# Performance work log

Measured on AMD Instinct MI355X. Metric: run time of the kernel, lower is better.

Reference implementation:

```python
import jax, jax.numpy as jnp
import numpy as np

B, N, C, HEADS = 8, 1024, 768, 12
HW = 32  # H = W = 32, so H*W == N


def _layernorm(x, g, b, eps=1e-5):
    mu = x.mean(-1, keepdims=True)
    var = ((x - mu) ** 2).mean(-1, keepdims=True)
    return (x - mu) * jax.lax.rsqrt(var + eps) * g + b


def setup_inputs() -> dict:
    key = jax.random.key(0)
    ks = jax.random.split(key, 6)
    w = lambda k, shape: jax.random.normal(k, shape, dtype=jnp.float32) * 0.02
    return {
        "x": jax.random.normal(ks[0], (B, N, C), dtype=jnp.float32),
        "y": jax.random.normal(ks[1], (B, C, HW, HW), dtype=jnp.float32),
        "q_w": w(ks[2], (C, C)),
        "q_b": jnp.zeros((C,), jnp.float32),
        "kv_w": w(ks[3], (2 * C, C)),
        "kv_b": jnp.zeros((2 * C,), jnp.float32),
        "proj_w": w(ks[4], (C, C)),
        "proj_b": jnp.zeros((C,), jnp.float32),
        "ln_g": jnp.ones((C,), jnp.float32),
        "ln_b": jnp.zeros((C,), jnp.float32),
        "H": HW,
        "W": HW,
    }


def reference(x, y, q_w, q_b, kv_w, kv_b, proj_w, proj_b, ln_g, ln_b, H, W):
    Bn, Nn, Cn = x.shape
    hd = Cn // HEADS
    scale = hd ** -0.5  # qk_scale=None, c_ratio=1 -> head_dim**-0.5

    # gating tensors from y
    y1 = y.reshape(Bn, Cn, H * W).transpose(0, 2, 1)          # [B, N, C]
    y2 = _layernorm(y1, ln_g, ln_b)
    yq = jax.nn.sigmoid(y2 @ q_w.T + q_b)                      # [B, N, C]
    ykv = jax.nn.sigmoid(y2 @ kv_w.T + kv_b)                   # [B, N, 2C]

    # gated q: q2 = q0 + q0*yq
    q0 = x @ q_w.T + q_b
    q = (q0 + q0 * yq).reshape(Bn, Nn, HEADS, hd).transpose(0, 2, 1, 3)  # [B,h,N,d]

    # gated kv: kv2 = kv0*ykv + ykv
    kv0 = x @ kv_w.T + kv_b
    kv = (kv0 * ykv + ykv).reshape(Bn, Nn, 2, HEADS, hd).transpose(2, 0, 3, 1, 4)
    k, v = kv[0], kv[1]                                        # [B,h,N,d] each

    attn = jax.nn.softmax(jnp.einsum("bhqd,bhkd->bhqk", q, k) * scale, axis=-1)
    out = jnp.einsum("bhqk,bhkd->bhqd", attn, v)
    out = out.transpose(0, 2, 1, 3).reshape(Bn, Nn, Cn)
    return out @ proj_w.T + proj_b
```

## Files before the change

kernel.cpp:

```cpp
#include <hip/hip_runtime.h>
#include <stdint.h>

typedef __attribute__((ext_vector_type(4))) float f4;
typedef __attribute__((ext_vector_type(8))) short bf16x8;
typedef __attribute__((ext_vector_type(4))) unsigned short u16x4;
typedef unsigned short u16;

#define B_ 8
#define N_ 1024
#define C_ 768
#define NH 12
#define HD 64

__device__ __forceinline__ float bf2f(u16 v) {
  union { unsigned u; float f; } x; x.u = ((unsigned)v) << 16; return x.f;
}
__device__ __forceinline__ u16 f2bf(float f) {
  union { float f; unsigned u; } x; x.f = f;
  unsigned r = x.u + 0x7FFFu + ((x.u >> 16) & 1u);
  return (u16)(r >> 16);
}
__device__ __forceinline__ void g2l16(const u16* g, const u16* l) {
  __builtin_amdgcn_global_load_lds(
      (const __attribute__((address_space(1))) void*)(uintptr_t)g,
      (__attribute__((address_space(3))) void*)(uint32_t)(uintptr_t)l,
      16, 0, 0);
}

#define SW6()  asm volatile("s_waitcnt vmcnt(6)" ::: "memory")
#define SW4()  asm volatile("s_waitcnt vmcnt(4)" ::: "memory")
#define SW3()  asm volatile("s_waitcnt vmcnt(3)" ::: "memory")
#define SW0()  asm volatile("s_waitcnt vmcnt(0)" ::: "memory")
#define BARF()                              \
  do {                                      \
    __builtin_amdgcn_s_barrier();           \
    asm volatile("" ::: "memory");          \
    __builtin_amdgcn_sched_barrier(0);      \
  } while (0)

__global__ __launch_bounds__(256) void cvt_bf16(const float* __restrict__ s,
                                                u16* __restrict__ d, int n4) {
  int i = blockIdx.x * 256 + threadIdx.x;
  int stride = gridDim.x * 256;
  for (; i < n4; i += stride) {
    float4 v = ((const float4*)s)[i];
    u16x4 o;
    o.x = f2bf(v.x); o.y = f2bf(v.y); o.z = f2bf(v.z); o.w = f2bf(v.w);
    ((u16x4*)d)[i] = o;
  }
}

__global__ __launch_bounds__(256) void ln_stats(const float* __restrict__ y,
                                                float* __restrict__ mu,
                                                float* __restrict__ rs,
                                                int b0) {
  __shared__ float s1[4][64], s2[4][64];
  int t = threadIdx.x;
  int nl = t & 63, ch = t >> 6;
  int idx0 = b0 * N_ + blockIdx.x * 64;
  int b = idx0 >> 10, nb_ = idx0 & 1023;
  const float* p = y + (size_t)b * C_ * N_ + nb_ + nl;
  float s = 0.f, q = 0.f;
  int c0 = ch * 192;
  for (int c = c0; c < c0 + 192; ++c) {
    float v = p[(size_t)c * N_];
    s += v; q += v * v;
  }
  s1[ch][nl] = s; s2[ch][nl] = q;
  __syncthreads();
  if (t < 64) {
    float ts = s1[0][t] + s1[1][t] + s1[2][t] + s1[3][t];
    float tq = s2[0][t] + s2[1][t] + s2[2][t] + s2[3][t];
    float m = ts * (1.f / C_);
    float var = tq * (1.f / C_) - m * m;
    mu[idx0 + t] = m;
    rs[idx0 + t] = rsqrtf(fmaxf(var, 0.f) + 1e-5f);
  }
}

__global__ __launch_bounds__(256) void ln_apply(const float* __restrict__ y,
                                                const float* __restrict__ mu,
                                                const float* __restrict__ rs,
                                                const float* __restrict__ lg,
                                                const float* __restrict__ lb,
                                                u16* __restrict__ y2c,
                                                int b0) {
  __shared__ float tile[64][65];
  int t = threadIdx.x;
  int n0 = blockIdx.x * 64, c0 = blockIdx.y * 64;
  int bl = blockIdx.z, b = b0 + bl;
  int jc = (t & 15) * 4, ir = t >> 4;
  for (int r = 0; r < 4; ++r) {
    int i = ir + r * 16;
    float4 v = *(const float4*)(y + ((size_t)b * C_ + c0 + i) * N_ + n0 + jc);
    tile[i][jc] = v.x; tile[i][jc + 1] = v.y; tile[i][jc + 2] = v.z; tile[i][jc + 3] = v.w;
  }
  __syncthreads();
  for (int r = 0; r < 4; ++r) {
    int i = ir + r * 16;
    int n = n0 + i;
    float m = mu[b * N_ + n], rr = rs[b * N_ + n];
    float g0 = lg[c0 + jc],     b0f = lb[c0 + jc];
    float g1 = lg[c0 + jc + 1], b1f = lb[c0 + jc + 1];
    float g2 = lg[c0 + jc + 2], b2f = lb[c0 + jc + 2];
    float g3 = lg[c0 + jc + 3], b3f = lb[c0 + jc + 3];
    u16x4 o;
    o.x = f2bf((tile[jc][i] - m) * rr * g0 + b0f);
    o.y = f2bf((tile[jc + 1][i] - m) * rr * g1 + b1f);
    o.z = f2bf((tile[jc + 2][i] - m) * rr * g2 + b2f);
    o.w = f2bf((tile[jc + 3][i] - m) * rr * g3 + b3f);
    *(u16x4*)(y2c + ((size_t)bl * N_ + n) * C_ + c0 + jc) = o;
  }
}

__global__ __launch_bounds__(256, 2) void gemm_gate(
    const u16* __restrict__ xbc, const u16* __restrict__ y2c,
    const u16* __restrict__ qwb, const u16* __restrict__ kvwb,
    const float* __restrict__ qb_, const float* __restrict__ kvb_,
    u16* __restrict__ o_q, u16* __restrict__ o_k, u16* __restrict__ o_vT) {
  __shared__ u16 smem[36864];
  int t = threadIdx.x, l = t & 63;
  int quad = l >> 4, l15 = l & 15;
  int w = t >> 6, wm = w & 1, wn = w >> 1;
  int m0l = blockIdx.x * 128;
  int n0l = blockIdx.y * 128;

  const u16* wp; const float* bp; int sel, h0;
  if (n0l < C_) {
    wp = qwb + (size_t)n0l * C_; bp = qb_ + n0l; sel = 0; h0 = n0l >> 6;
  } else {
    int nk = n0l - C_;
    wp = kvwb + (size_t)nk * C_; bp = kvb_ + nk;
    sel = (nk < C_) ? 1 : 2;
    h0 = ((sel == 2) ? nk - C_ : nk) >> 6;
  }

  f4 accx[4][4], accy[4][4];
  for (int i = 0; i < 4; ++i)
    for (int j = 0; j < 4; ++j) {
      accx[i][j] = (f4){0.f, 0.f, 0.f, 0.f};
      accy[i][j] = (f4){0.f, 0.f, 0.f, 0.f};
    }

  int row = t >> 2;
  int colS = (((t & 3) ^ (row & 3)) * 8);
  const u16* gx = xbc + (size_t)(m0l + row) * C_ + colS;
  const u16* gy = y2c + (size_t)(m0l + row) * C_ + colS;
  const u16* gw = wp + (size_t)row * C_ + colS;
  int rsl = (quad ^ (l15 & 3)) * 8;

#define STAGE_G(OFF, kk)                                   \
  do {                                                     \
    u16* p_ = smem + (OFF);                                \
    g2l16(gx + (kk),           p_ + t * 8);                \
    g2l16(gx + (kk) + 64 * C_, p_ + 2048 + t * 8);         \
    g2l16(gy + (kk),           p_ + 4096 + t * 8);         \
    g2l16(gy + (kk) + 64 * C_, p_ + 6144 + t * 8);         \
    g2l16(gw + (kk),           p_ + 8192 + t * 8);         \
    g2l16(gw + (kk) + 64 * C_, p_ + 10240 + t * 8);        \
  } while (0)

#define COMPUTE_G(OFF)                                                        \
  do {                                                                        \
    const u16* base = smem + (OFF);                                           \
    bf16x8 afx[4], afy[4], bfr[4];                                            \
    for (int i = 0; i < 4; ++i) {                                             \
      int ra = (wm * 64 + i * 16 + l15) * 32 + rsl;                           \
      afx[i] = *(const bf16x8*)&base[ra];                                     \
      afy[i] = *(const bf16x8*)&base[4096 + ra];                              \
      int rb = (wn * 64 + i * 16 + l15) * 32 + rsl;                           \
      bfr[i] = *(const bf16x8*)&base[8192 + rb];                              \
    }                                                                         \
    for (int i = 0; i < 4; ++i)                                               \
      for (int j = 0; j < 4; ++j) {                                           \
        accx[i][j] = __builtin_amdgcn_mfma_f32_16x16x32_bf16(afx[i], bfr[j], accx[i][j], 0, 0, 0); \
        accy[i][j] = __builtin_amdgcn_mfma_f32_16x16x32_bf16(afy[i], bfr[j], accy[i][j], 0, 0, 0); \
      }                                                                       \
  } while (0)

#define STEP_G(i, OFFC, OFFS)                                 \
  do {                                                        \
    if ((i) <= 21) STAGE_G(OFFS, ((i) + 2) * 32);             \
    COMPUTE_G(OFFC);                                          \
    if ((i) <= 21)      SW6();                                \
    else if ((i) == 22) SW0();                                \
    BARF();                                                   \
  } while (0)

  STAGE_G(0, 0);
  STAGE_G(12288, 32);
  SW6();
  BARF();
  for (int n = 0; n < 24; n += 3) {
    STEP_G(n,     0,     24576);
    STEP_G(n + 1, 12288, 0);
    STEP_G(n + 2, 24576, 12288);
  }
#undef STEP_G
#undef STAGE_G
#undef COMPUTE_G

  const int PITCH = 136;
  for (int j = 0; j < 4; ++j) {
    int cloc = wn * 64 + j * 16 + l15;
    float bias = bp[cloc];
    for (int i = 0; i < 4; ++i) {
      int rb0 = wm * 64 + i * 16 + quad * 4;
      for (int r = 0; r < 4; ++r) {
        int rloc = rb0 + r;
        float vx = accx[i][j][r] + bias;
        float vy = accy[i][j][r] + bias;
        float gg = 1.f / (1.f + __expf(-vy));
        float val = (sel == 0) ? vx * (1.f + gg) : gg * (vx + 1.f);
        u16 bv = f2bf(val);
        if (sel == 2) smem[cloc * PITCH + rloc] = bv;
        else          smem[rloc * PITCH + cloc] = bv;
      }
    }
  }
  __syncthreads();
  {
    int rr = t >> 1, hh = t & 1;
    const u16* src = smem + rr * PITCH + hh * 64;
    u16* dst;
    if (sel == 2) {
      int h = h0 + (rr >> 6), d = rr & 63;
      int bl = m0l >> 10, nbase = m0l & 1023;
      dst = o_vT + (size_t)((bl * NH + h) * HD + d) * N_ + nbase + hh * 64;
    } else {
      int gml = m0l + rr;
      int bl = gml >> 10, n = gml & 1023;
      int h = h0 + hh;
      dst = (sel == 0 ? o_q : o_k) + (size_t)((bl * NH + h) * N_ + n) * HD;
    }
    for (int c = 0; c < 8; ++c) {
      bf16x8 v = *(const bf16x8*)(src + c * 8);
      *(bf16x8*)(dst + c * 8) = v;
    }
  }
}

__global__ __launch_bounds__(256) void attn(const u16* __restrict__ qoc,
                                            const u16* __restrict__ koc,
                                            const u16* __restrict__ vTc,
                                            u16* __restrict__ aoc) {
  __shared__ u16 Qs[4096], Ks[8192], Vs[8192];
  __shared__ u16 Ps[64 * 72];
  int t = threadIdx.x, l = t & 63, w = t >> 6;
  int quad = l >> 4, l15 = l & 15;
  int bhl = blockIdx.y;
  int bl = bhl / NH, h = bhl % NH;
  int q0 = blockIdx.x * 64;
  int sr = t >> 3;
  int swo = ((t & 7) ^ (sr & 7)) * 8;
  const u16* qbp = qoc + ((size_t)bhl * N_ + q0) * HD;
  const u16* kb = koc + (size_t)bhl * N_ * HD;
  const u16* vb = vTc + (size_t)bhl * HD * N_;

#define STAGE_KV(OFF, key0)                                                   \
  do {                                                                        \
    g2l16(kb + (size_t)((key0) + sr) * HD + swo,      Ks + (OFF) + t * 8);    \
    g2l16(kb + (size_t)((key0) + 32 + sr) * HD + swo, Ks + (OFF) + 2048 + t * 8); \
    g2l16(vb + (size_t)sr * N_ + (key0) + swo,        Vs + (OFF) + t * 8);    \
    g2l16(vb + (size_t)(32 + sr) * N_ + (key0) + swo, Vs + (OFF) + 2048 + t * 8); \
  } while (0)

  g2l16(qbp + sr * HD + swo,        Qs + t * 8);
  g2l16(qbp + (32 + sr) * HD + swo, Qs + 2048 + t * 8);
  STAGE_KV(0, 0);
  STAGE_KV(4096, 64);
  SW4();
  BARF();

  int sA = (quad ^ (l15 & 7)) * 8;
  int sB = sA ^ 32;
  bf16x8 aq0 = *(const bf16x8*)&Qs[(w * 16 + l15) * 64 + sA];
  bf16x8 aq1 = *(const bf16x8*)&Qs[(w * 16 + l15) * 64 + sB];
  f4 o[4];
  for (int i = 0; i < 4; ++i) o[i] = (f4){0.f, 0.f, 0.f, 0.f};
  f4 ls = (f4){0.f, 0.f, 0.f, 0.f};
  bf16x8 ones;
  for (int i = 0; i < 8; ++i) ones[i] = (short)0x3F80;

#define TILE_STEP(KOFF)                                                       \
  do {                                                                        \
    f4 s_[4];                                                                 \
    __builtin_amdgcn_s_setprio(1);                                            \
    for (int ni = 0; ni < 4; ++ni) {                                          \
      bf16x8 b0v = *(const bf16x8*)&Ks[(KOFF) + (ni * 16 + l15) * 64 + sA];   \
      bf16x8 b1v = *(const bf16x8*)&Ks[(KOFF) + (ni * 16 + l15) * 64 + sB];   \
      f4 z = (f4){0.f, 0.f, 0.f, 0.f};                                        \
      z = __builtin_amdgcn_mfma_f32_16x16x32_bf16(aq0, b0v, z, 0, 0, 0);      \
      z = __builtin_amdgcn_mfma_f32_16x16x32_bf16(aq1, b1v, z, 0, 0, 0);      \
      s_[ni] = z;                                                             \
    }                                                                         \
    __builtin_amdgcn_s_setprio(0);                                            \
    for (int ni = 0; ni < 4; ++ni)                                            \
      for (int r = 0; r < 4; ++r)                                             \
        Ps[(w * 16 + quad * 4 + r) * 72 + ni * 16 + l15] =                    \
            f2bf(__expf(s_[ni][r] * 0.125f));                                 \
    bf16x8 ap0 = *(const bf16x8*)&Ps[(w * 16 + l15) * 72 + quad * 8];         \
    bf16x8 ap1 = *(const bf16x8*)&Ps[(w * 16 + l15) * 72 + 32 + quad * 8];    \
    __builtin_amdgcn_s_setprio(1);                                            \
    for (int ni = 0; ni < 4; ++ni) {                                          \
      bf16x8 b0v = *(const bf16x8*)&Vs[(KOFF) + (ni * 16 + l15) * 64 + sA];   \
      bf16x8 b1v = *(const bf16x8*)&Vs[(KOFF) + (ni * 16 + l15) * 64 + sB];   \
      o[ni] = __builtin_amdgcn_mfma_f32_16x16x32_bf16(ap0, b0v, o[ni], 0, 0, 0); \
      o[ni] = __builtin_amdgcn_mfma_f32_16x16x32_bf16(ap1, b1v, o[ni], 0, 0, 0); \
    }                                                                         \
    ls = __builtin_amdgcn_mfma_f32_16x16x32_bf16(ap0, ones, ls, 0, 0, 0);     \
    ls = __builtin_amdgcn_mfma_f32_16x16x32_bf16(ap1, ones, ls, 0, 0, 0);     \
    __builtin_amdgcn_s_setprio(0);                                            \
  } while (0)

  for (int kt = 0; kt < 16; kt += 2) {
    TILE_STEP(0);
    BARF();
    if (kt + 2 < 16) { STAGE_KV(0, (kt + 2) * 64); SW4(); } else { SW0(); }
    BARF();
    TILE_STEP(4096);
    BARF();
    if (kt + 3 < 16) { STAGE_KV(4096, (kt + 3) * 64); SW4(); } else { SW0(); }
    BARF();
  }
#undef TILE_STEP
#undef STAGE_KV

  for (int ni = 0; ni < 4; ++ni)
    for (int r = 0; r < 4; ++r)
      Ps[(w * 16 + quad * 4 + r) * 72 + ni * 16 + l15] =
          f2bf(o[ni][r] / ls[r]);
  __syncthreads();
  {
    int rr = t >> 2, cc = t & 3;
    int n = q0 + rr;
    const u16* src = Ps + rr * 72 + cc * 16;
    u16* dst = aoc + ((size_t)bl * N_ + n) * C_ + h * HD + cc * 16;
    *(bf16x8*)dst = *(const bf16x8*)src;
    *(bf16x8*)(dst + 8) = *(const bf16x8*)(src + 8);
  }
}

__global__ __launch_bounds__(256, 2) void gemm_proj(const u16* __restrict__ aoc,
                                                    const u16* __restrict__ pwb,
                                                    const float* __restrict__ bias,
                                                    float* __restrict__ out,
                                                    int b0) {
  __shared__ u16 smem[18432];
  int t = threadIdx.x, l = t & 63;
  int quad = l >> 4, l15 = l & 15;
  int w = t >> 6, wm = w & 1, wn = w >> 1;
  int m0l = blockIdx.x * 128, n0 = blockIdx.y * 64;
  f4 acc[4][2];
  for (int i = 0; i < 4; ++i)
    for (int j = 0; j < 2; ++j) acc[i][j] = (f4){0.f, 0.f, 0.f, 0.f};
  int row = t >> 2;
  int colS = (((t & 3) ^ (row & 3)) * 8);
  const u16* ga = aoc + (size_t)(m0l + row) * C_ + colS;
  const u16* gw = pwb + (size_t)(n0 + row) * C_ + colS;
  int rsl = (quad ^ (l15 & 3)) * 8;

#define STAGE_P(OFF, kk)                                   \
  do {                                                     \
    u16* p_ = smem + (OFF);                                \
    g2l16(ga + (kk),           p_ + t * 8);                \
    g2l16(ga + (kk) + 64 * C_, p_ + 2048 + t * 8);         \
    g2l16(gw + (kk),           p_ + 4096 + t * 8);         \
  } while (0)

#define COMPUTE_P(OFF)                                                        \
  do {                                                                        \
    const u16* base = smem + (OFF);                                           \
    bf16x8 af[4], bfr[2];                                                     \
    for (int i = 0; i < 4; ++i)                                               \
      af[i] = *(const bf16x8*)&base[(wm * 64 + i * 16 + l15) * 32 + rsl];     \
    for (int j = 0; j < 2; ++j)                                               \
      bfr[j] = *(const bf16x8*)&base[4096 + (wn * 32 + j * 16 + l15) * 32 + rsl]; \
    for (int i = 0; i < 4; ++i)                                               \
      for (int j = 0; j < 2; ++j)                                             \
        acc[i][j] = __builtin_amdgcn_mfma_f32_16x16x32_bf16(af[i], bfr[j], acc[i][j], 0, 0, 0); \
  } while (0)

#define STEP_P(i, OFFC, OFFS)                                 \
  do {                                                        \
    if ((i) <= 21) STAGE_P(OFFS, ((i) + 2) * 32);             \
    COMPUTE_P(OFFC);                                          \
    if ((i) <= 21)      SW3();                                \
    else if ((i) == 22) SW0();                                \
    BARF();                                                   \
  } while (0)

  STAGE_P(0, 0);
  STAGE_P(6144, 32);
  SW3();
  BARF();
  for (int n = 0; n < 24; n += 3) {
    STEP_P(n,     0,     12288);
    STEP_P(n + 1, 6144,  0);
    STEP_P(n + 2, 12288, 6144);
  }
#undef STEP_P
#undef STAGE_P
#undef COMPUTE_P

  for (int j = 0; j < 2; ++j) {
    int gcol = n0 + wn * 32 + j * 16 + l15;
    float bv = bias[gcol];
    for (int i = 0; i < 4; ++i) {
      int rbase = m0l + wm * 64 + i * 16 + quad * 4;
      for (int r = 0; r < 4; ++r)
        __builtin_nontemporal_store(acc[i][j][r] + bv,
                                    &out[(size_t)(b0 * N_ + rbase + r) * C_ + gcol]);
    }
  }
}

extern "C" void kernel_launch(void* const* d_in, const int* in_sizes, int n_in,
                              void* d_out, int out_size, void* d_ws, size_t ws_size,
                              hipStream_t stream) {
  const float* x   = (const float*)d_in[0];
  const float* y   = (const float*)d_in[1];
  const float* qw  = (const float*)d_in[2];
  const float* qb  = (const float*)d_in[3];
  const float* kvw = (const float*)d_in[4];
  const float* kvb = (const float*)d_in[5];
  const float* pw  = (const float*)d_in[6];
  const float* pb  = (const float*)d_in[7];
  const float* lg  = (const float*)d_in[8];
  const float* lb  = (const float*)d_in[9];

  char* ws = (char*)d_ws;
  float* mu = (float*)(ws);
  float* rs = (float*)(ws + 32768);
  u16* qwb  = (u16*)(ws + 65536);
  u16* kvwb = (u16*)(ws + 1245184);
  u16* pwb  = (u16*)(ws + 3604480);
  const size_t BASE2 = 4784128;
  const size_t PER_B = 1572864;

  int nb = 1;
  for (int c = 8; c >= 1; c >>= 1) {
    if (BASE2 + 5 * (size_t)c * PER_B <= ws_size) { nb = c; break; }
  }
  u16* xbc = (u16*)(ws + BASE2);
  u16* y2c = (u16*)(ws + BASE2 + (size_t)nb * PER_B);
  u16* qoc = (u16*)(ws + BASE2 + 2 * (size_t)nb * PER_B);
  u16* koc = (u16*)(ws + BASE2 + 3 * (size_t)nb * PER_B);
  u16* vTc = (u16*)(ws + BASE2 + 4 * (size_t)nb * PER_B);
  u16* aoc = xbc;

  cvt_bf16<<<dim3(576), dim3(256), 0, stream>>>(qw, qwb, 147456);
  cvt_bf16<<<dim3(1152), dim3(256), 0, stream>>>(kvw, kvwb, 294912);
  cvt_bf16<<<dim3(576), dim3(256), 0, stream>>>(pw, pwb, 147456);

  for (int b0 = 0; b0 < B_; b0 += nb) {
    cvt_bf16<<<dim3(768 * nb), dim3(256), 0, stream>>>(
        x + (size_t)b0 * N_ * C_, xbc, nb * 196608);
    ln_stats<<<dim3(16 * nb), dim3(256), 0, stream>>>(y, mu, rs, b0);
    ln_apply<<<dim3(16, 12, nb), dim3(256), 0, stream>>>(y, mu, rs, lg, lb, y2c, b0);
    gemm_gate<<<dim3(8 * nb, 18), dim3(256), 0, stream>>>(xbc, y2c, qwb, kvwb,
                                                          qb, kvb, qoc, koc, vTc);
    attn<<<dim3(16, 12 * nb), dim3(256), 0, stream>>>(qoc, koc, vTc, aoc);
    gemm_proj<<<dim3(8 * nb, 12), dim3(256), 0, stream>>>(aoc, pwb, pb, (float*)d_out, b0);
  }
}
```

Measured before the change: 285.5 us.

## Shrink gate GEMM N-tile to 64 and drop triple-buffered LDS pipeline

```diff
diff --git a/kernel.cpp b/kernel.cpp
--- a/kernel.cpp
+++ b/kernel.cpp
@@ -27,7 +27,6 @@
       16, 0, 0);
 }
 
-#define SW6()  asm volatile("s_waitcnt vmcnt(6)" ::: "memory")
 #define SW4()  asm volatile("s_waitcnt vmcnt(4)" ::: "memory")
 #define SW3()  asm volatile("s_waitcnt vmcnt(3)" ::: "memory")
 #define SW0()  asm volatile("s_waitcnt vmcnt(0)" ::: "memory")
@@ -113,17 +112,17 @@
   }
 }
 
-__global__ __launch_bounds__(256, 2) void gemm_gate(
+__global__ __launch_bounds__(256, 4) void gemm_gate(
     const u16* __restrict__ xbc, const u16* __restrict__ y2c,
     const u16* __restrict__ qwb, const u16* __restrict__ kvwb,
     const float* __restrict__ qb_, const float* __restrict__ kvb_,
     u16* __restrict__ o_q, u16* __restrict__ o_k, u16* __restrict__ o_vT) {
-  __shared__ u16 smem[36864];
+  __shared__ u16 smem[10240];
   int t = threadIdx.x, l = t & 63;
   int quad = l >> 4, l15 = l & 15;
   int w = t >> 6, wm = w & 1, wn = w >> 1;
   int m0l = blockIdx.x * 128;
-  int n0l = blockIdx.y * 128;
+  int n0l = blockIdx.y * 64;
 
   const u16* wp; const float* bp; int sel, h0;
   if (n0l < C_) {
@@ -135,74 +134,50 @@
     h0 = ((sel == 2) ? nk - C_ : nk) >> 6;
   }
 
-  f4 accx[4][4], accy[4][4];
+  f4 accx[4][2], accy[4][2];
   for (int i = 0; i < 4; ++i)
-    for (int j = 0; j < 4; ++j) {
+    for (int j = 0; j < 2; ++j) {
       accx[i][j] = (f4){0.f, 0.f, 0.f, 0.f};
       accy[i][j] = (f4){0.f, 0.f, 0.f, 0.f};
     }
 
-  int row = t >> 2;
-  int colS = (((t & 3) ^ (row & 3)) * 8);
-  const u16* gx = xbc + (size_t)(m0l + row) * C_ + colS;
-  const u16* gy = y2c + (size_t)(m0l + row) * C_ + colS;
-  const u16* gw = wp + (size_t)row * C_ + colS;
-  int rsl = (quad ^ (l15 & 3)) * 8;
-
-#define STAGE_G(OFF, kk)                                   \
-  do {                                                     \
-    u16* p_ = smem + (OFF);                                \
-    g2l16(gx + (kk),           p_ + t * 8);                \
-    g2l16(gx + (kk) + 64 * C_, p_ + 2048 + t * 8);         \
-    g2l16(gy + (kk),           p_ + 4096 + t * 8);         \
-    g2l16(gy + (kk) + 64 * C_, p_ + 6144 + t * 8);         \
-    g2l16(gw + (kk),           p_ + 8192 + t * 8);         \
-    g2l16(gw + (kk) + 64 * C_, p_ + 10240 + t * 8);        \
-  } while (0)
-
-#define COMPUTE_G(OFF)                                                        \
-  do {                                                                        \
-    const u16* base = smem + (OFF);                                           \
-    bf16x8 afx[4], afy[4], bfr[4];                                            \
-    for (int i = 0; i < 4; ++i) {                                             \
-      int ra = (wm * 64 + i * 16 + l15) * 32 + rsl;                           \
-      afx[i] = *(const bf16x8*)&base[ra];                                     \
-      afy[i] = *(const bf16x8*)&base[4096 + ra];                              \
-      int rb = (wn * 64 + i * 16 + l15) * 32 + rsl;                           \
-      bfr[i] = *(const bf16x8*)&base[8192 + rb];                              \
-    }                                                                         \
-    for (int i = 0; i < 4; ++i)                                               \
-      for (int j = 0; j < 4; ++j) {                                           \
-        accx[i][j] = __builtin_amdgcn_mfma_f32_16x16x32_bf16(afx[i], bfr[j], accx[i][j], 0, 0, 0); \
-        accy[i][j] = __builtin_amdgcn_mfma_f32_16x16x32_bf16(afy[i], bfr[j], accy[i][j], 0, 0, 0); \
-      }                                                                       \
-  } while (0)
-
-#define STEP_G(i, OFFC, OFFS)                                 \
-  do {                                                        \
-    if ((i) <= 21) STAGE_G(OFFS, ((i) + 2) * 32);             \
-    COMPUTE_G(OFFC);                                          \
-    if ((i) <= 21)      SW6();                                \
-    else if ((i) == 22) SW0();                                \
-    BARF();                                                   \
-  } while (0)
-
-  STAGE_G(0, 0);
-  STAGE_G(12288, 32);
-  SW6();
-  BARF();
-  for (int n = 0; n < 24; n += 3) {
-    STEP_G(n,     0,     24576);
-    STEP_G(n + 1, 12288, 0);
-    STEP_G(n + 2, 24576, 12288);
-  }
-#undef STEP_G
-#undef STAGE_G
-#undef COMPUTE_G
-
-  const int PITCH = 136;
-  for (int j = 0; j < 4; ++j) {
-    int cloc = wn * 64 + j * 16 + l15;
+  int row = t >> 2, colb = (t & 3) * 8;
+  const u16* gx = xbc + (size_t)(m0l + row) * C_ + colb;
+  const u16* gy = y2c + (size_t)(m0l + row) * C_ + colb;
+  const u16* gw = wp + (size_t)row * C_ + colb;
+
+  for (int kk = 0; kk < C_; kk += 32) {
+    __syncthreads();
+    g2l16(gx + kk,           smem + t * 8);
+    g2l16(gx + kk + 64 * C_, smem + 2048 + t * 8);
+    g2l16(gy + kk,           smem + 4096 + t * 8);
+    g2l16(gy + kk + 64 * C_, smem + 6144 + t * 8);
+    g2l16(gw + kk,           smem + 8192 + t * 8);
+    __syncthreads();
+    bf16x8 bfr[2];
+    for (int j = 0; j < 2; ++j)
+      bfr[j] = *(const bf16x8*)&smem[8192 + (wn * 32 + j * 16 + l15) * 32 + quad * 8];
+    {
+      bf16x8 afx[4];
+      for (int i = 0; i < 4; ++i)
+        afx[i] = *(const bf16x8*)&smem[(wm * 64 + i * 16 + l15) * 32 + quad * 8];
+      for (int i = 0; i < 4; ++i)
+        for (int j = 0; j < 2; ++j)
+          accx[i][j] = __builtin_amdgcn_mfma_f32_16x16x32_bf16(afx[i], bfr[j], accx[i][j], 0, 0, 0);
+    }
+    {
+      bf16x8 afy[4];
+      for (int i = 0; i < 4; ++i)
+        afy[i] = *(const bf16x8*)&smem[4096 + (wm * 64 + i * 16 + l15) * 32 + quad * 8];
+      for (int i = 0; i < 4; ++i)
+        for (int j = 0; j < 2; ++j)
+          accy[i][j] = __builtin_amdgcn_mfma_f32_16x16x32_bf16(afy[i], bfr[j], accy[i][j], 0, 0, 0);
+    }
+  }
+
+  __syncthreads();
+  for (int j = 0; j < 2; ++j) {
+    int cloc = wn * 32 + j * 16 + l15;
     float bias = bp[cloc];
     for (int i = 0; i < 4; ++i) {
       int rb0 = wm * 64 + i * 16 + quad * 4;
@@ -213,29 +188,29 @@
         float gg = 1.f / (1.f + __expf(-vy));
         float val = (sel == 0) ? vx * (1.f + gg) : gg * (vx + 1.f);
         u16 bv = f2bf(val);
-        if (sel == 2) smem[cloc * PITCH + rloc] = bv;
-        else          smem[rloc * PITCH + cloc] = bv;
+        if (sel == 2) smem[cloc * 136 + rloc] = bv;
+        else          smem[rloc * 72 + cloc] = bv;
       }
     }
   }
   __syncthreads();
   {
-    int rr = t >> 1, hh = t & 1;
-    const u16* src = smem + rr * PITCH + hh * 64;
-    u16* dst;
+    int bl = m0l >> 10, nbase = m0l & 1023;
     if (sel == 2) {
-      int h = h0 + (rr >> 6), d = rr & 63;
-      int bl = m0l >> 10, nbase = m0l & 1023;
-      dst = o_vT + (size_t)((bl * NH + h) * HD + d) * N_ + nbase + hh * 64;
+      int d = t >> 2, qc = t & 3;
+      const u16* src = smem + d * 136 + qc * 32;
+      u16* dst = o_vT + (size_t)((bl * NH + h0) * HD + d) * N_ + nbase + qc * 32;
+      for (int c = 0; c < 4; ++c)
+        *(bf16x8*)(dst + c * 8) = *(const bf16x8*)(src + c * 8);
     } else {
+      int rr = t >> 1, hf = t & 1;
+      const u16* src = smem + rr * 72 + hf * 32;
       int gml = m0l + rr;
-      int bl = gml >> 10, n = gml & 1023;
-      int h = h0 + hh;
-      dst = (sel == 0 ? o_q : o_k) + (size_t)((bl * NH + h) * N_ + n) * HD;
-    }
-    for (int c = 0; c < 8; ++c) {
-      bf16x8 v = *(const bf16x8*)(src + c * 8);
-      *(bf16x8*)(dst + c * 8) = v;
+      int bl2 = gml >> 10, n = gml & 1023;
+      u16* dst = (sel == 0 ? o_q : o_k) +
+                 (size_t)((bl2 * NH + h0) * N_ + n) * HD + hf * 32;
+      for (int c = 0; c < 4; ++c)
+        *(bf16x8*)(dst + c * 8) = *(const bf16x8*)(src + c * 8);
     }
   }
 }
@@ -458,7 +433,7 @@
         x + (size_t)b0 * N_ * C_, xbc, nb * 196608);
     ln_stats<<<dim3(16 * nb), dim3(256), 0, stream>>>(y, mu, rs, b0);
     ln_apply<<<dim3(16, 12, nb), dim3(256), 0, stream>>>(y, mu, rs, lg, lb, y2c, b0);
-    gemm_gate<<<dim3(8 * nb, 18), dim3(256), 0, stream>>>(xbc, y2c, qwb, kvwb,
+    gemm_gate<<<dim3(8 * nb, 36), dim3(256), 0, stream>>>(xbc, y2c, qwb, kvwb,
                                                           qb, kvb, qoc, koc, vTc);
     attn<<<dim3(16, 12 * nb), dim3(256), 0, stream>>>(qoc, koc, vTc, aoc);
     gemm_proj<<<dim3(8 * nb, 12), dim3(256), 0, stream>>>(aoc, pwb, pb, (float*)d_out, b0);
```

New measurement: 301.1 us. 5.5% more time.
